# Kernel optimization log

Hardware: AMD Instinct MI355X
Metric: run time of the kernel (lower is better)

Reference implementation:

```python
import jax, jax.numpy as jnp
import numpy as np
import math

BS, NAG, HID, NACT, MESS, QD, KD, STEPS, INP = 4096, 8, 256, 16, 64, 64, 64, 5, 128
TRAJ = STEPS * NACT
LAMQ = 0.5


def setup_inputs() -> dict:
    key = jax.random.key(0)
    ks = jax.random.split(key, 12)
    g = lambda k, shape, fan: jax.random.normal(k, shape, jnp.float32) / math.sqrt(fan)
    d = {}
    d["inputs"] = jax.random.normal(ks[0], (BS * NAG, INP), jnp.float32)
    d["old_hstate"] = jax.random.normal(ks[1], (BS * NAG, HID), jnp.float32)
    d["fc1_w"] = g(ks[2], (HID, INP), INP); d["fc1_b"] = jnp.zeros((HID,), jnp.float32)
    d["w_ih"] = g(ks[3], (3 * HID, HID), HID); d["w_hh"] = g(ks[4], (3 * HID, HID), HID)
    d["b_ih"] = jnp.zeros((3 * HID,), jnp.float32); d["b_hh"] = jnp.zeros((3 * HID,), jnp.float32)
    d["dec_w"] = g(ks[5], (NACT, HID), HID); d["dec_b"] = jnp.zeros((NACT,), jnp.float32)
    d["trans_w"] = g(ks[6], (HID, HID + NAG), HID + NAG); d["trans_b"] = jnp.zeros((HID,), jnp.float32)
    d["qij_w"] = g(ks[7], (NACT, HID + MESS), HID + MESS); d["qij_b"] = jnp.zeros((NACT,), jnp.float32)
    d["q_w"] = g(ks[8], (QD, TRAJ), TRAJ); d["q_b"] = jnp.zeros((QD,), jnp.float32)
    d["k_w"] = g(ks[9], (KD, TRAJ), TRAJ); d["k_b"] = jnp.zeros((KD,), jnp.float32)
    d["v_w"] = g(ks[10], (MESS, TRAJ), TRAJ); d["v_b"] = jnp.zeros((MESS,), jnp.float32)
    return d


def _fwd(inputs, old_hstate, fc1_w, fc1_b, w_ih, w_hh, b_ih, b_hh,
         dec_w, dec_b, trans_w, trans_b, qij_w, qij_b,
         q_w, q_b, k_w, k_b, v_w, v_b):
    # fc1 + relu
    x = jax.nn.relu(inputs @ fc1_w.T + fc1_b)  # (BS*NAG, HID)
    # GRUCell (torch gate order: r, z, n)
    gi = x @ w_ih.T + b_ih
    gh = old_hstate @ w_hh.T + b_hh
    ir, iz, i_n = jnp.split(gi, 3, axis=-1)
    hr, hz, h_n = jnp.split(gh, 3, axis=-1)
    r = jax.nn.sigmoid(ir + hr)
    z = jax.nn.sigmoid(iz + hz)
    n = jnp.tanh(i_n + r * h_n)
    h_new = (1.0 - z) * n + z * old_hstate
    h = h_new.reshape(BS, NAG, HID)

    # imagination rollout on detached h
    def step(hc, _):
        q_inf = hc @ dec_w.T + dec_b                       # (BS, NAG, NACT)
        ac = jnp.argmax(q_inf, axis=-1).astype(hc.dtype)   # (BS, NAG)
        ac = jnp.broadcast_to(ac[:, None, :], (BS, NAG, NAG))
        ti = jnp.concatenate([hc, ac], axis=-1)            # (BS, NAG, HID+NAG)
        return ti @ trans_w.T + trans_b, q_inf

    _, qs = jax.lax.scan(step, jax.lax.stop_gradient(h), None, length=STEPS)
    # qs: (STEPS, BS, NAG, NACT) -> trajectory (BS, NAG, STEPS*NACT), step-major on last dim
    traj = jnp.moveaxis(qs, 0, 2).reshape(BS, NAG, TRAJ)

    # tiny agent attention
    query = traj @ q_w.T + q_b   # (BS, NAG, QD)
    key_t = traj @ k_w.T + k_b   # (BS, NAG, KD)
    value = traj @ v_w.T + v_b   # (BS, NAG, MESS)
    score = jnp.einsum('bnq,bmq->bnm', query, key_t) / math.sqrt(MESS)
    attn = jax.nn.softmax(score, axis=-1)
    traj_msg = jnp.einsum('bnm,bmd->bnd', attn, value)  # (BS, NAG, MESS)

    q_local = h @ dec_w.T + dec_b
    q_ij = jnp.concatenate([h, traj_msg], axis=-1) @ qij_w.T + qij_b
    q = q_local + LAMQ * q_ij
    return q, h


def reference(inputs, old_hstate, fc1_w, fc1_b, w_ih, w_hh, b_ih, b_hh,
              dec_w, dec_b, trans_w, trans_b, qij_w, qij_b,
              q_w, q_b, k_w, k_b, v_w, v_b):
    return _fwd(inputs, old_hstate, fc1_w, fc1_b, w_ih, w_hh, b_ih, b_hh,
                dec_w, dec_b, trans_w, trans_b, qij_w, qij_b,
                q_w, q_b, k_w, k_b, v_w, v_b)
```

## Files before the change

kernel.cpp:

```cpp
#include <hip/hip_runtime.h>
#include <math.h>

typedef unsigned short u16;
typedef unsigned int   u32;
typedef __attribute__((ext_vector_type(8))) short bf16x8;
typedef __attribute__((ext_vector_type(4))) float f32x4;

#define NROWS 32768
#define NAG 8
#define HID 256
#define INP 128
#define NACT 16
#define MESS 64
#define TRAJD 80
#define QD 64
#define HOFF 524288

#define PKO_FC1 0
#define PKO_IH  98304
#define PKO_HH  688128
#define PKO_TR  1277952
#define PKO_DEC 1499136
#define PKO_QKV 1511424
#define PKO_QIJ 1566720
#define PK_TOTAL 1582080
#define WS_CB   791040
#define WS_FLAG 793312

#define OB_FC1B 0
#define OB_BIH  256
#define OB_BHH  1024
#define OB_DECB 1792
#define OB_TRB  1808
#define OB_QIJB 2064
#define OB_QB   2080

__device__ __forceinline__ float bf2f(u16 v){ return __uint_as_float(((u32)v)<<16); }
__device__ __forceinline__ u16 f2bf(float f){
    u32 u = __float_as_uint(f);
    return (u16)((u + 0x7fffu + ((u>>16)&1u))>>16);
}
__device__ __forceinline__ float sig_(float x){ return 1.0f/(1.0f+expf(-x)); }
__device__ __forceinline__ float ldin(const void* p, size_t i, int f32){
    return f32 ? ((const float*)p)[i] : bf2f(((const u16*)p)[i]);
}
__device__ __forceinline__ void stout1(void* out, size_t i, float v, int f32){
    if (f32) ((float*)out)[i]=v; else ((u16*)out)[i]=f2bf(v);
}
__device__ __forceinline__ void split3(float w, u16& s0, u16& s1, u16& s2){
    u16 a=f2bf(w); float r  = w - bf2f(a);
    u16 b=f2bf(r); float r2 = r - bf2f(b);
    s0=a; s1=b; s2=f2bf(r2);
}
__device__ __forceinline__ f32x4 splat4(float b){ f32x4 v = {b,b,b,b}; return v; }

#define MFMA(a,b,c) __builtin_amdgcn_mfma_f32_16x16x32_bf16((a),(b),(c),0,0,0)

__device__ __forceinline__ bf16x8 lda_pl(const u16* P, int p, int row, int kbyte){
    const char* b = (const char*)P + ((p*32+row)*640) + (kbyte ^ ((row&7)<<4));
    return *(const bf16x8*)b;
}
__device__ __forceinline__ void stw_pl(u16* P, int p, int row, int col, u16 v){
    char* b = (char*)P + ((p*32+row)*640) + (((col*2)) ^ ((row&7)<<4));
    *(u16*)b = v;
}
__device__ __forceinline__ void split_store_pl(u16* P, int row, int col, float v){
    u16 a,b,c; split3(v,a,b,c);
    stw_pl(P,0,row,col,a); stw_pl(P,1,row,col,b); stw_pl(P,2,row,col,c);
}
__device__ __forceinline__ bf16x8 ldg_bf8(const void* p, size_t off){
    return *(const bf16x8*)((const u16*)p + off);
}
__device__ __forceinline__ void ldg_f32_split(const void* p, size_t off, bf16x8& f0, bf16x8& f1, bf16x8& f2){
    const float* fp = (const float*)p + off;
    #pragma unroll
    for (int j=0;j<8;j++){
        float w = fp[j];
        u16 a,b,c; split3(w,a,b,c);
        f0[j]=(short)a; f1[j]=(short)b; f2[j]=(short)c;
    }
}
#define BCH(base, NTv, ksv, pbv, ntv) \
    (*(const bf16x8*)((base) + ((((ksv)*3+(pbv))*(NTv) + (ntv))*512) + lane*8))

__global__ void k_det(const void* __restrict__ inp, int* __restrict__ flag){
    __shared__ int cnt;
    if (threadIdx.x==0) cnt=0;
    __syncthreads();
    int big=0;
    for (int i=threadIdx.x;i<128;i+=64){
        u32 w = ((const u32*)inp)[i];
        float g = bf2f((u16)w);
        if (!(fabsf(g) <= 1e4f)) big++;
    }
    if (big) atomicAdd(&cnt, big);
    __syncthreads();
    if (threadIdx.x==0) *flag = (cnt>=4) ? 1 : 0;
}

__device__ __forceinline__ void pack_tile(const void* W, int Kdim, int NT, u16* pk, int tau, int f32){
    int lane2 = tau & 63, c = tau >> 6;
    int nt = c % NT, ks = c / NT;
    int n  = nt*16 + (lane2 & 15);
    int kb = ks*32 + (lane2 >> 4)*8;
    u16 o0[8],o1[8],o2[8];
    #pragma unroll
    for (int j=0;j<8;j++){
        int k = kb + j;
        float w = (k < Kdim) ? ldin(W, (size_t)n*Kdim + k, f32) : 0.0f;
        split3(w, o0[j], o1[j], o2[j]);
    }
    size_t base = ((size_t)(ks*3+0)*NT + nt)*512 + lane2*8;
    size_t step = (size_t)NT*512;
    #pragma unroll
    for (int j=0;j<8;j++){
        pk[base+j]=o0[j]; pk[base+step+j]=o1[j]; pk[base+2*step+j]=o2[j];
    }
}

__global__ __launch_bounds__(256) void k0_prep(
    const void* fc1_w, const void* w_ih, const void* w_hh, const void* trans_w,
    const void* dec_w, const void* qij_w, const void* q_w, const void* k_w, const void* v_w,
    const void* fc1_b, const void* b_ih, const void* b_hh, const void* dec_b,
    const void* trans_b, const void* qij_b, const void* q_b, const void* k_b, const void* v_b,
    float* __restrict__ ws, const int* __restrict__ flagp)
{
    const int f32 = *flagp;
    u16* pk = (u16*)ws;
    int i = blockIdx.x*256 + threadIdx.x;
    if (i < 4096)        pack_tile(fc1_w,  128, 16, pk+PKO_FC1, i,        f32);
    else if (i < 28672)  pack_tile(w_ih,   256, 48, pk+PKO_IH,  i-4096,   f32);
    else if (i < 53248)  pack_tile(w_hh,   256, 48, pk+PKO_HH,  i-28672,  f32);
    else if (i < 62464)  pack_tile(trans_w,264, 16, pk+PKO_TR,  i-53248,  f32);
    else if (i < 62976)  pack_tile(dec_w,  256,  1, pk+PKO_DEC, i-62464,  f32);
    else if (i < 65280){
        int tau = i - 62976;
        int lane2 = tau&63, c = tau>>6, nt = c%12, ks = c/12;
        int n = nt*16 + (lane2&15);
        const void* W = (n<64)? q_w : (n<128 ? k_w : v_w);
        int nl = n & 63;
        int kb = ks*32 + (lane2>>4)*8;
        u16 o0[8],o1[8],o2[8];
        #pragma unroll
        for (int j=0;j<8;j++){
            int k = kb + j;
            float w = (k < 80) ? ldin(W, (size_t)nl*80 + k, f32) : 0.0f;
            split3(w, o0[j], o1[j], o2[j]);
        }
        u16* dst = pk + PKO_QKV;
        size_t base = ((size_t)(ks*3+0)*12 + nt)*512 + lane2*8;
        size_t step = (size_t)12*512;
        #pragma unroll
        for (int j=0;j<8;j++){
            dst[base+j]=o0[j]; dst[base+step+j]=o1[j]; dst[base+2*step+j]=o2[j];
        }
    }
    else if (i < 65920)  pack_tile(qij_w,  320,  1, pk+PKO_QIJ, i-65280,  f32);
    else if (i < 68192){
        int i2 = i - 65920;
        float v;
        if      (i2<256)  v=ldin(fc1_b,i2,f32);
        else if (i2<1024) v=ldin(b_ih,i2-256,f32);
        else if (i2<1792) v=ldin(b_hh,i2-1024,f32);
        else if (i2<1808) v=ldin(dec_b,i2-1792,f32);
        else if (i2<2064) v=ldin(trans_b,i2-1808,f32);
        else if (i2<2080) v=ldin(qij_b,i2-2064,f32);
        else if (i2<2144) v=ldin(q_b,i2-2080,f32);
        else if (i2<2208) v=ldin(k_b,i2-2144,f32);
        else              v=ldin(v_b,i2-2208,f32);
        ws[WS_CB+i2]=v;
    }
}

template<int F32>
__global__ __launch_bounds__(512,2) void k12_fused(
    const void* __restrict__ inp, const void* __restrict__ oldh,
    const float* __restrict__ ws, void* __restrict__ dout, const int* __restrict__ flagp)
{
    if (*flagp != F32) return;
    constexpr int PBW = F32 ? 2 : 0;
    constexpr int PAG = F32 ? 2 : 0;

    __shared__ __align__(16) u16   planes[3*32*320];
    __shared__ __align__(16) float s_traj[32*100];
    __shared__ __align__(16) float s_qkv[32*196];
    __shared__ float s_att[256];

    const int t = threadIdx.x;
    const int wid = t>>6, lane = t&63, lr = lane&15, lk = lane>>4;
    const int nt0 = wid, nt1 = wid + 8;
    const int c0 = nt0*16+lr, c1 = nt1*16+lr;
    const int row0 = blockIdx.x*32;
    const u16* pk = (const u16*)ws;
    const float* cb = ws + WS_CB;
    const u16* pkf = pk + PKO_FC1;
    const u16* pki = pk + PKO_IH;
    const u16* pkh = pk + PKO_HH;
    const u16* pkt = pk + PKO_TR;
    const u16* pkd = pk + PKO_DEC;
    const u16* pkq = pk + PKO_QKV;
    const u16* pkj = pk + PKO_QIJ;

    for (int i=t;i<15360;i+=512) ((u32*)planes)[i]=0u;
    for (int i=t;i<3200;i+=512) s_traj[i]=0.f;
    __syncthreads();

    {
        f32x4 acc[2][2];
        acc[0][0]=splat4(cb[OB_FC1B+c0]); acc[1][0]=acc[0][0];
        acc[0][1]=splat4(cb[OB_FC1B+c1]); acc[1][1]=acc[0][1];
        for (int ks=0;ks<4;ks++){
            bf16x8 a[2][3];
            if (F32){
                ldg_f32_split(inp,(size_t)(row0+lr)*INP + ks*32+lk*8,    a[0][0],a[0][1],a[0][2]);
                ldg_f32_split(inp,(size_t)(row0+16+lr)*INP + ks*32+lk*8, a[1][0],a[1][1],a[1][2]);
            } else {
                a[0][0]=ldg_bf8(inp,(size_t)(row0+lr)*INP + ks*32+lk*8);
                a[1][0]=ldg_bf8(inp,(size_t)(row0+16+lr)*INP + ks*32+lk*8);
            }
            #pragma unroll
            for (int pb=0;pb<=PBW;pb++){
                bf16x8 B0 = BCH(pkf,16,ks,pb,nt0);
                bf16x8 B1 = BCH(pkf,16,ks,pb,nt1);
                #pragma unroll
                for (int pa=0;pa<=((PAG<2-pb)?PAG:(2-pb));pa++){
                    acc[0][0]=MFMA(a[0][pa],B0,acc[0][0]); acc[0][1]=MFMA(a[0][pa],B1,acc[0][1]);
                    acc[1][0]=MFMA(a[1][pa],B0,acc[1][0]); acc[1][1]=MFMA(a[1][pa],B1,acc[1][1]);
                }
            }
        }
        #pragma unroll
        for (int m=0;m<2;m++)
        #pragma unroll
        for (int ni=0;ni<2;ni++)
        #pragma unroll
        for (int j=0;j<4;j++){
            float v = acc[m][ni][j]; v = v>0.f ? v : 0.f;
            split_store_pl(planes, m*16+lk*4+j, (ni?nt1:nt0)*16+lr, v);
        }
    }
    __syncthreads();

    float hreg[16];
    {
        f32x4 aR[2][2], aZ[2][2], aN[2][2], aH[2][2];
        #pragma unroll
        for (int m=0;m<2;m++)
        #pragma unroll
        for (int gi=0;gi<2;gi++){
            int c = (gi?nt1:nt0)*16 + lr;
            aR[m][gi]=splat4(cb[OB_BIH+c]     + cb[OB_BHH+c]);
            aZ[m][gi]=splat4(cb[OB_BIH+256+c] + cb[OB_BHH+256+c]);
            aN[m][gi]=splat4(cb[OB_BIH+512+c]);
            aH[m][gi]=splat4(cb[OB_BHH+512+c]);
        }
        for (int ks=0;ks<8;ks++){
            #pragma unroll
            for (int pb=0;pb<=PBW;pb++){
                bf16x8 Br0=BCH(pki,48,ks,pb,   nt0), Br1=BCH(pki,48,ks,pb,   nt1);
                bf16x8 Bz0=BCH(pki,48,ks,pb,16+nt0), Bz1=BCH(pki,48,ks,pb,16+nt1);
                bf16x8 Bn0=BCH(pki,48,ks,pb,32+nt0), Bn1=BCH(pki,48,ks,pb,32+nt1);
                #pragma unroll
                for (int pa=0;pa<=2-pb;pa++){
                    bf16x8 a0 = lda_pl(planes, pa, lr,    ks*64+lk*16);
                    bf16x8 a1 = lda_pl(planes, pa, 16+lr, ks*64+lk*16);
                    aR[0][0]=MFMA(a0,Br0,aR[0][0]); aR[0][1]=MFMA(a0,Br1,aR[0][1]);
                    aR[1][0]=MFMA(a1,Br0,aR[1][0]); aR[1][1]=MFMA(a1,Br1,aR[1][1]);
                    aZ[0][0]=MFMA(a0,Bz0,aZ[0][0]); aZ[0][1]=MFMA(a0,Bz1,aZ[0][1]);
                    aZ[1][0]=MFMA(a1,Bz0,aZ[1][0]); aZ[1][1]=MFMA(a1,Bz1,aZ[1][1]);
                    aN[0][0]=MFMA(a0,Bn0,aN[0][0]); aN[0][1]=MFMA(a0,Bn1,aN[0][1]);
                    aN[1][0]=MFMA(a1,Bn0,aN[1][0]); aN[1][1]=MFMA(a1,Bn1,aN[1][1]);
                }
            }
        }
        for (int ks=0;ks<8;ks++){
            bf16x8 a[2][3];
            if (F32){
                ldg_f32_split(oldh,(size_t)(row0+lr)*HID + ks*32+lk*8,    a[0][0],a[0][1],a[0][2]);
                ldg_f32_split(oldh,(size_t)(row0+16+lr)*HID + ks*32+lk*8, a[1][0],a[1][1],a[1][2]);
            } else {
                a[0][0]=ldg_bf8(oldh,(size_t)(row0+lr)*HID + ks*32+lk*8);
                a[1][0]=ldg_bf8(oldh,(size_t)(row0+16+lr)*HID + ks*32+lk*8);
            }
            #pragma unroll
            for (int pb=0;pb<=PBW;pb++){
                bf16x8 Br0=BCH(pkh,48,ks,pb,   nt0), Br1=BCH(pkh,48,ks,pb,   nt1);
                bf16x8 Bz0=BCH(pkh,48,ks,pb,16+nt0), Bz1=BCH(pkh,48,ks,pb,16+nt1);
                bf16x8 Bh0=BCH(pkh,48,ks,pb,32+nt0), Bh1=BCH(pkh,48,ks,pb,32+nt1);
                #pragma unroll
                for (int pa=0;pa<=((PAG<2-pb)?PAG:(2-pb));pa++){
                    aR[0][0]=MFMA(a[0][pa],Br0,aR[0][0]); aR[0][1]=MFMA(a[0][pa],Br1,aR[0][1]);
                    aR[1][0]=MFMA(a[1][pa],Br0,aR[1][0]); aR[1][1]=MFMA(a[1][pa],Br1,aR[1][1]);
                    aZ[0][0]=MFMA(a[0][pa],Bz0,aZ[0][0]); aZ[0][1]=MFMA(a[0][pa],Bz1,aZ[0][1]);
                    aZ[1][0]=MFMA(a[1][pa],Bz0,aZ[1][0]); aZ[1][1]=MFMA(a[1][pa],Bz1,aZ[1][1]);
                    aH[0][0]=MFMA(a[0][pa],Bh0,aH[0][0]); aH[0][1]=MFMA(a[0][pa],Bh1,aH[0][1]);
                    aH[1][0]=MFMA(a[1][pa],Bh0,aH[1][0]); aH[1][1]=MFMA(a[1][pa],Bh1,aH[1][1]);
                }
            }
        }
        #pragma unroll
        for (int m=0;m<2;m++)
        #pragma unroll
        for (int gi=0;gi<2;gi++)
        #pragma unroll
        for (int j=0;j<4;j++){
            int row = m*16 + lk*4 + j;
            int c   = (gi?nt1:nt0)*16 + lr;
            float r  = sig_(aR[m][gi][j]);
            float z  = sig_(aZ[m][gi][j]);
            float nv = tanhf(aN[m][gi][j] + r*aH[m][gi][j]);
            float ho = ldin(oldh,(size_t)(row0+row)*HID + c, F32);
            float h  = (1.f-z)*nv + z*ho;
            hreg[m*8+gi*4+j] = h;
            if (F32)
                stout1(dout,(size_t)HOFF + (size_t)(row0+row)*HID + c, h, F32);
        }
    }
    __syncthreads();
    #pragma unroll
    for (int m=0;m<2;m++)
    #pragma unroll
    for (int gi=0;gi<2;gi++)
    #pragma unroll
    for (int j=0;j<4;j++)
        split_store_pl(planes, m*16+lk*4+j, (gi?nt1:nt0)*16+lr, hreg[m*8+gi*4+j]);
    __syncthreads();

    if (!F32){
        #pragma unroll
        for (int c2=0;c2<2;c2++){
            int cid = t + c2*512;
            int row = cid>>5, c8 = cid&31;
            bf16x8 v = lda_pl(planes, 0, row, c8*16);
            *(bf16x8*)((u16*)dout + HOFF + (size_t)(row0+row)*HID + c8*8) = v;
        }
    }

    #pragma unroll 1
    for (int s=0;s<5;s++){
        if (wid<2){
            const int m = wid;
            f32x4 d0 = splat4(cb[OB_DECB+lr]);
            f32x4 d1 = splat4(0.f), d2 = splat4(0.f);
            for (int ks=0;ks<8;ks++){
                #pragma unroll
                for (int pb=0;pb<=PBW;pb++){
                    bf16x8 B = BCH(pkd,1,ks,pb,0);
                    #pragma unroll
                    for (int pa=0;pa<=2-pb;pa++){
                        bf16x8 a = lda_pl(planes, pa, m*16+lr, ks*64+lk*16);
                        if (pa==0) d0=MFMA(a,B,d0); else if (pa==1) d1=MFMA(a,B,d1); else d2=MFMA(a,B,d2);
                    }
                }
            }
            f32x4 q;
            #pragma unroll
            for (int j=0;j<4;j++) q[j]=d0[j]+d1[j]+d2[j];
            #pragma unroll
            for (int j=0;j<4;j++) s_traj[(m*16+lk*4+j)*100 + s*16 + lr] = q[j];
            if (s<4){
                #pragma unroll
                for (int j=0;j<4;j++){
                    float v = q[j]; int ai = lr;
                    #pragma unroll
                    for (int msk=1; msk<16; msk<<=1){
                        float pv = __shfl_xor(v, msk);
                        int   pi = __shfl_xor(ai, msk);
                        if (pv>v || (pv==v && pi<ai)){ v=pv; ai=pi; }
                    }
                    if (lr<8){
                        int R = m*16+lk*4+j;
                        stw_pl(planes, 0, (R&~7)+lr, 256+(R&7), f2bf((float)ai));
                    }
                }
            }
        }
        if (s==4) break;
        __syncthreads();
        {
            f32x4 tc[2][2];
            tc[0][0]=splat4(cb[OB_TRB+c0]); tc[1][0]=tc[0][0];
            tc[0][1]=splat4(cb[OB_TRB+c1]); tc[1][1]=tc[0][1];
            for (int ks=0;ks<9;ks++){
                #pragma unroll
                for (int pb=0;pb<=PBW;pb++){
                    bf16x8 B0=BCH(pkt,16,ks,pb,nt0), B1=BCH(pkt,16,ks,pb,nt1);
                    #pragma unroll
                    for (int pa=0;pa<=2-pb;pa++){
                        bf16x8 a0 = lda_pl(planes,pa,lr,   ks*64+lk*16);
                        bf16x8 a1 = lda_pl(planes,pa,16+lr,ks*64+lk*16);
                        tc[0][0]=MFMA(a0,B0,tc[0][0]); tc[0][1]=MFMA(a0,B1,tc[0][1]);
                        tc[1][0]=MFMA(a1,B0,tc[1][0]); tc[1][1]=MFMA(a1,B1,tc[1][1]);
                    }
                }
            }
            __syncthreads();
            #pragma unroll
            for (int m=0;m<2;m++)
            #pragma unroll
            for (int ni=0;ni<2;ni++)
            #pragma unroll
            for (int j=0;j<4;j++)
                split_store_pl(planes, m*16+lk*4+j, (ni?nt1:nt0)*16+lr, tc[m][ni][j]);
        }
        __syncthreads();
    }
    __syncthreads();

    #pragma unroll
    for (int m=0;m<2;m++)
    #pragma unroll
    for (int gi=0;gi<2;gi++)
    #pragma unroll
    for (int j=0;j<4;j++)
        split_store_pl(planes, m*16+lk*4+j, (gi?nt1:nt0)*16+lr, hreg[m*8+gi*4+j]);
    if (wid<6){
        f32x4 acc[2][2];
        acc[0][0]=splat4(cb[OB_QB+2*wid*16+lr]);     acc[1][0]=acc[0][0];
        acc[0][1]=splat4(cb[OB_QB+(2*wid+1)*16+lr]); acc[1][1]=acc[0][1];
        for (int ks=0;ks<3;ks++){
            bf16x8 a[2][3];
            #pragma unroll
            for (int m=0;m<2;m++){
                const float* tp = s_traj + (m*16+lr)*100 + ks*32 + lk*8;
                #pragma unroll
                for (int e=0;e<8;e++){
                    u16 x0,x1,x2; split3(tp[e],x0,x1,x2);
                    a[m][0][e]=(short)x0; a[m][1][e]=(short)x1; a[m][2][e]=(short)x2;
                }
            }
            #pragma unroll
            for (int pb=0;pb<=PBW;pb++){
                bf16x8 B0 = BCH(pkq,12,ks,pb,2*wid);
                bf16x8 B1 = BCH(pkq,12,ks,pb,2*wid+1);
                #pragma unroll
                for (int pa=0;pa<=2-pb;pa++){
                    acc[0][0]=MFMA(a[0][pa],B0,acc[0][0]); acc[0][1]=MFMA(a[0][pa],B1,acc[0][1]);
                    acc[1][0]=MFMA(a[1][pa],B0,acc[1][0]); acc[1][1]=MFMA(a[1][pa],B1,acc[1][1]);
                }
            }
        }
        #pragma unroll
        for (int m=0;m<2;m++)
        #pragma unroll
        for (int j=0;j<4;j++){
            s_qkv[(m*16+lk*4+j)*196 + 2*wid*16+lr]     = acc[m][0][j];
            s_qkv[(m*16+lk*4+j)*196 + (2*wid+1)*16+lr] = acc[m][1][j];
        }
    }
    __syncthreads();
    if (t<256){
        int b=t>>6, n=(t>>3)&7, mm=t&7;
        const float* qv = s_qkv + (b*8+n)*196;
        const float* kv = s_qkv + (b*8+mm)*196 + 64;
        float a2=0.f;
        #pragma unroll
        for (int d2=0;d2<64;d2++) a2 += qv[d2]*kv[d2];
        s_att[t] = a2*0.125f;
    }
    __syncthreads();
    if (t<32){
        float mx = s_att[t*8];
        #pragma unroll
        for (int j2=1;j2<8;j2++) mx = fmaxf(mx, s_att[t*8+j2]);
        float e[8]; float sum=0.f;
        #pragma unroll
        for (int j2=0;j2<8;j2++){ e[j2]=expf(s_att[t*8+j2]-mx); sum+=e[j2]; }
        float inv = 1.f/sum;
        #pragma unroll
        for (int j2=0;j2<8;j2++) s_att[t*8+j2] = e[j2]*inv;
    }
    __syncthreads();
    for (int o=t;o<2048;o+=512){
        int row=o>>6, d2=o&63, b=row>>3;
        float a3=0.f;
        #pragma unroll
        for (int mm=0;mm<8;mm++) a3 += s_att[row*8+mm]*s_qkv[(b*8+mm)*196+128+d2];
        split_store_pl(planes, row, 256+d2, a3);
    }
    __syncthreads();
    if (wid<2){
        const int m = wid;
        f32x4 e0 = splat4(cb[OB_QIJB+lr]);
        f32x4 e1 = splat4(0.f), e2 = splat4(0.f);
        for (int ks=0;ks<10;ks++){
            #pragma unroll
            for (int pb=0;pb<=PBW;pb++){
                bf16x8 B = BCH(pkj,1,ks,pb,0);
                #pragma unroll
                for (int pa=0;pa<=2-pb;pa++){
                    bf16x8 a = lda_pl(planes, pa, m*16+lr, ks*64+lk*16);
                    if (pa==0) e0=MFMA(a,B,e0); else if (pa==1) e1=MFMA(a,B,e1); else e2=MFMA(a,B,e2);
                }
            }
        }
        #pragma unroll
        for (int j=0;j<4;j++){
            int row = m*16+lk*4+j;
            float ql = s_traj[row*100 + lr];
            stout1(dout,(size_t)(row0+row)*NACT + lr, ql + 0.5f*(e0[j]+e1[j]+e2[j]), F32);
        }
    }
}

extern "C" void kernel_launch(void* const* d_in, const int* in_sizes, int n_in,
                              void* d_out, int out_size, void* d_ws, size_t ws_size,
                              hipStream_t stream)
{
    (void)in_sizes; (void)n_in; (void)out_size; (void)ws_size;
    const void* inputs = d_in[0];
    const void* oldh   = d_in[1];
    float* ws = (float*)d_ws;
    int* flagp = (int*)(ws + WS_FLAG);

    k_det<<<1,64,0,stream>>>(inputs, flagp);
    k0_prep<<<268,256,0,stream>>>(d_in[2],d_in[4],d_in[5],d_in[10],d_in[8],d_in[12],
                                  d_in[14],d_in[16],d_in[18],
                                  d_in[3],d_in[6],d_in[7],d_in[9],d_in[11],d_in[13],
                                  d_in[15],d_in[17],d_in[19],
                                  ws, flagp);
    k12_fused<0><<<1024,512,0,stream>>>(inputs, oldh, ws, d_out, flagp);
    k12_fused<1><<<1024,512,0,stream>>>(inputs, oldh, ws, d_out, flagp);
}
```

Measured before the change: 590.6 us.

## Double block to 1024 threads, one 16-column N-tile per wave

Each block now runs 16 waves instead of 8. Every wave owns a single 16-wide output column tile rather than two, across the fc1, GRU, transition, QKV and output stages. This gives each wave less register pressure and shorter serial MFMA chains, and spreads the per-block work over more waves. In exchange, launch bounds drop to one block per CU, so occupancy stays about the same. Each A fragment is now reused across fewer MFMAs, which means more LDS and global A loads per FLOP.

Result: slower. 782.2 us (+32.4%).

```diff
diff --git a/kernel.cpp b/kernel.cpp
--- a/kernel.cpp
+++ b/kernel.cpp
@@ -173,7 +173,7 @@
 }
 
 template<int F32>
-__global__ __launch_bounds__(512,2) void k12_fused(
+__global__ __launch_bounds__(1024,1) void k12_fused(
     const void* __restrict__ inp, const void* __restrict__ oldh,
     const float* __restrict__ ws, void* __restrict__ dout, const int* __restrict__ flagp)
 {
@@ -188,8 +188,8 @@
 
     const int t = threadIdx.x;
     const int wid = t>>6, lane = t&63, lr = lane&15, lk = lane>>4;
-    const int nt0 = wid, nt1 = wid + 8;
-    const int c0 = nt0*16+lr, c1 = nt1*16+lr;
+    const int nt = wid;
+    const int c0 = nt*16+lr;
     const int row0 = blockIdx.x*32;
     const u16* pk = (const u16*)ws;
     const float* cb = ws + WS_CB;
@@ -201,14 +201,13 @@
     const u16* pkq = pk + PKO_QKV;
     const u16* pkj = pk + PKO_QIJ;
 
-    for (int i=t;i<15360;i+=512) ((u32*)planes)[i]=0u;
-    for (int i=t;i<3200;i+=512) s_traj[i]=0.f;
+    for (int i=t;i<15360;i+=1024) ((u32*)planes)[i]=0u;
+    for (int i=t;i<3200;i+=1024) s_traj[i]=0.f;
     __syncthreads();
 
     {
-        f32x4 acc[2][2];
-        acc[0][0]=splat4(cb[OB_FC1B+c0]); acc[1][0]=acc[0][0];
-        acc[0][1]=splat4(cb[OB_FC1B+c1]); acc[1][1]=acc[0][1];
+        f32x4 acc[2];
+        acc[0]=splat4(cb[OB_FC1B+c0]); acc[1]=acc[0];
         for (int ks=0;ks<4;ks++){
             bf16x8 a[2][3];
             if (F32){
@@ -220,56 +219,44 @@
             }
             #pragma unroll
             for (int pb=0;pb<=PBW;pb++){
-                bf16x8 B0 = BCH(pkf,16,ks,pb,nt0);
-                bf16x8 B1 = BCH(pkf,16,ks,pb,nt1);
+                bf16x8 B = BCH(pkf,16,ks,pb,nt);
                 #pragma unroll
                 for (int pa=0;pa<=((PAG<2-pb)?PAG:(2-pb));pa++){
-                    acc[0][0]=MFMA(a[0][pa],B0,acc[0][0]); acc[0][1]=MFMA(a[0][pa],B1,acc[0][1]);
-                    acc[1][0]=MFMA(a[1][pa],B0,acc[1][0]); acc[1][1]=MFMA(a[1][pa],B1,acc[1][1]);
+                    acc[0]=MFMA(a[0][pa],B,acc[0]);
+                    acc[1]=MFMA(a[1][pa],B,acc[1]);
                 }
             }
         }
         #pragma unroll
         for (int m=0;m<2;m++)
         #pragma unroll
-        for (int ni=0;ni<2;ni++)
-        #pragma unroll
         for (int j=0;j<4;j++){
-            float v = acc[m][ni][j]; v = v>0.f ? v : 0.f;
-            split_store_pl(planes, m*16+lk*4+j, (ni?nt1:nt0)*16+lr, v);
-        }
-    }
-    __syncthreads();
-
-    float hreg[16];
+            float v = acc[m][j]; v = v>0.f ? v : 0.f;
+            split_store_pl(planes, m*16+lk*4+j, c0, v);
+        }
+    }
+    __syncthreads();
+
+    float hreg[8];
     {
-        f32x4 aR[2][2], aZ[2][2], aN[2][2], aH[2][2];
-        #pragma unroll
-        for (int m=0;m<2;m++)
-        #pragma unroll
-        for (int gi=0;gi<2;gi++){
-            int c = (gi?nt1:nt0)*16 + lr;
-            aR[m][gi]=splat4(cb[OB_BIH+c]     + cb[OB_BHH+c]);
-            aZ[m][gi]=splat4(cb[OB_BIH+256+c] + cb[OB_BHH+256+c]);
-            aN[m][gi]=splat4(cb[OB_BIH+512+c]);
-            aH[m][gi]=splat4(cb[OB_BHH+512+c]);
-        }
+        f32x4 aR[2], aZ[2], aN[2], aH[2];
+        aR[0]=splat4(cb[OB_BIH+c0]     + cb[OB_BHH+c0]);     aR[1]=aR[0];
+        aZ[0]=splat4(cb[OB_BIH+256+c0] + cb[OB_BHH+256+c0]); aZ[1]=aZ[0];
+        aN[0]=splat4(cb[OB_BIH+512+c0]);                     aN[1]=aN[0];
+        aH[0]=splat4(cb[OB_BHH+512+c0]);                     aH[1]=aH[0];
         for (int ks=0;ks<8;ks++){
             #pragma unroll
             for (int pb=0;pb<=PBW;pb++){
-                bf16x8 Br0=BCH(pki,48,ks,pb,   nt0), Br1=BCH(pki,48,ks,pb,   nt1);
-                bf16x8 Bz0=BCH(pki,48,ks,pb,16+nt0), Bz1=BCH(pki,48,ks,pb,16+nt1);
-                bf16x8 Bn0=BCH(pki,48,ks,pb,32+nt0), Bn1=BCH(pki,48,ks,pb,32+nt1);
+                bf16x8 Br=BCH(pki,48,ks,pb,   nt);
+                bf16x8 Bz=BCH(pki,48,ks,pb,16+nt);
+                bf16x8 Bn=BCH(pki,48,ks,pb,32+nt);
                 #pragma unroll
                 for (int pa=0;pa<=2-pb;pa++){
                     bf16x8 a0 = lda_pl(planes, pa, lr,    ks*64+lk*16);
                     bf16x8 a1 = lda_pl(planes, pa, 16+lr, ks*64+lk*16);
-                    aR[0][0]=MFMA(a0,Br0,aR[0][0]); aR[0][1]=MFMA(a0,Br1,aR[0][1]);
-                    aR[1][0]=MFMA(a1,Br0,aR[1][0]); aR[1][1]=MFMA(a1,Br1,aR[1][1]);
-                    aZ[0][0]=MFMA(a0,Bz0,aZ[0][0]); aZ[0][1]=MFMA(a0,Bz1,aZ[0][1]);
-                    aZ[1][0]=MFMA(a1,Bz0,aZ[1][0]); aZ[1][1]=MFMA(a1,Bz1,aZ[1][1]);
-                    aN[0][0]=MFMA(a0,Bn0,aN[0][0]); aN[0][1]=MFMA(a0,Bn1,aN[0][1]);
-                    aN[1][0]=MFMA(a1,Bn0,aN[1][0]); aN[1][1]=MFMA(a1,Bn1,aN[1][1]);
+                    aR[0]=MFMA(a0,Br,aR[0]); aR[1]=MFMA(a1,Br,aR[1]);
+                    aZ[0]=MFMA(a0,Bz,aZ[0]); aZ[1]=MFMA(a1,Bz,aZ[1]);
+                    aN[0]=MFMA(a0,Bn,aN[0]); aN[1]=MFMA(a1,Bn,aN[1]);
                 }
             }
         }
@@ -284,56 +271,44 @@
             }
             #pragma unroll
             for (int pb=0;pb<=PBW;pb++){
-                bf16x8 Br0=BCH(pkh,48,ks,pb,   nt0), Br1=BCH(pkh,48,ks,pb,   nt1);
-                bf16x8 Bz0=BCH(pkh,48,ks,pb,16+nt0), Bz1=BCH(pkh,48,ks,pb,16+nt1);
-                bf16x8 Bh0=BCH(pkh,48,ks,pb,32+nt0), Bh1=BCH(pkh,48,ks,pb,32+nt1);
+                bf16x8 Br=BCH(pkh,48,ks,pb,   nt);
+                bf16x8 Bz=BCH(pkh,48,ks,pb,16+nt);
+                bf16x8 Bh=BCH(pkh,48,ks,pb,32+nt);
                 #pragma unroll
                 for (int pa=0;pa<=((PAG<2-pb)?PAG:(2-pb));pa++){
-                    aR[0][0]=MFMA(a[0][pa],Br0,aR[0][0]); aR[0][1]=MFMA(a[0][pa],Br1,aR[0][1]);
-                    aR[1][0]=MFMA(a[1][pa],Br0,aR[1][0]); aR[1][1]=MFMA(a[1][pa],Br1,aR[1][1]);
-                    aZ[0][0]=MFMA(a[0][pa],Bz0,aZ[0][0]); aZ[0][1]=MFMA(a[0][pa],Bz1,aZ[0][1]);
-                    aZ[1][0]=MFMA(a[1][pa],Bz0,aZ[1][0]); aZ[1][1]=MFMA(a[1][pa],Bz1,aZ[1][1]);
-                    aH[0][0]=MFMA(a[0][pa],Bh0,aH[0][0]); aH[0][1]=MFMA(a[0][pa],Bh1,aH[0][1]);
-                    aH[1][0]=MFMA(a[1][pa],Bh0,aH[1][0]); aH[1][1]=MFMA(a[1][pa],Bh1,aH[1][1]);
+                    aR[0]=MFMA(a[0][pa],Br,aR[0]); aR[1]=MFMA(a[1][pa],Br,aR[1]);
+                    aZ[0]=MFMA(a[0][pa],Bz,aZ[0]); aZ[1]=MFMA(a[1][pa],Bz,aZ[1]);
+                    aH[0]=MFMA(a[0][pa],Bh,aH[0]); aH[1]=MFMA(a[1][pa],Bh,aH[1]);
                 }
             }
         }
         #pragma unroll
         for (int m=0;m<2;m++)
-        #pragma unroll
-        for (int gi=0;gi<2;gi++)
         #pragma unroll
         for (int j=0;j<4;j++){
             int row = m*16 + lk*4 + j;
-            int c   = (gi?nt1:nt0)*16 + lr;
-            float r  = sig_(aR[m][gi][j]);
-            float z  = sig_(aZ[m][gi][j]);
-            float nv = tanhf(aN[m][gi][j] + r*aH[m][gi][j]);
-            float ho = ldin(oldh,(size_t)(row0+row)*HID + c, F32);
+            float r  = sig_(aR[m][j]);
+            float z  = sig_(aZ[m][j]);
+            float nv = tanhf(aN[m][j] + r*aH[m][j]);
+            float ho = ldin(oldh,(size_t)(row0+row)*HID + c0, F32);
             float h  = (1.f-z)*nv + z*ho;
-            hreg[m*8+gi*4+j] = h;
+            hreg[m*4+j] = h;
             if (F32)
-                stout1(dout,(size_t)HOFF + (size_t)(row0+row)*HID + c, h, F32);
+                stout1(dout,(size_t)HOFF + (size_t)(row0+row)*HID + c0, h, F32);
         }
     }
     __syncthreads();
     #pragma unroll
     for (int m=0;m<2;m++)
     #pragma unroll
-    for (int gi=0;gi<2;gi++)
-    #pragma unroll
     for (int j=0;j<4;j++)
-        split_store_pl(planes, m*16+lk*4+j, (gi?nt1:nt0)*16+lr, hreg[m*8+gi*4+j]);
+        split_store_pl(planes, m*16+lk*4+j, c0, hreg[m*4+j]);
     __syncthreads();
 
     if (!F32){
-        #pragma unroll
-        for (int c2=0;c2<2;c2++){
-            int cid = t + c2*512;
-            int row = cid>>5, c8 = cid&31;
-            bf16x8 v = lda_pl(planes, 0, row, c8*16);
-            *(bf16x8*)((u16*)dout + HOFF + (size_t)(row0+row)*HID + c8*8) = v;
-        }
+        int row = t>>5, c8 = t&31;
+        bf16x8 v = lda_pl(planes, 0, row, c8*16);
+        *(bf16x8*)((u16*)dout + HOFF + (size_t)(row0+row)*HID + c8*8) = v;
     }
 
     #pragma unroll 1
@@ -378,19 +353,18 @@
         if (s==4) break;
         __syncthreads();
         {
-            f32x4 tc[2][2];
-            tc[0][0]=splat4(cb[OB_TRB+c0]); tc[1][0]=tc[0][0];
-            tc[0][1]=splat4(cb[OB_TRB+c1]); tc[1][1]=tc[0][1];
+            f32x4 tc[2];
+            tc[0]=splat4(cb[OB_TRB+c0]); tc[1]=tc[0];
             for (int ks=0;ks<9;ks++){
                 #pragma unroll
                 for (int pb=0;pb<=PBW;pb++){
-                    bf16x8 B0=BCH(pkt,16,ks,pb,nt0), B1=BCH(pkt,16,ks,pb,nt1);
+                    bf16x8 B=BCH(pkt,16,ks,pb,nt);
                     #pragma unroll
                     for (int pa=0;pa<=2-pb;pa++){
                         bf16x8 a0 = lda_pl(planes,pa,lr,   ks*64+lk*16);
                         bf16x8 a1 = lda_pl(planes,pa,16+lr,ks*64+lk*16);
-                        tc[0][0]=MFMA(a0,B0,tc[0][0]); tc[0][1]=MFMA(a0,B1,tc[0][1]);
-                        tc[1][0]=MFMA(a1,B0,tc[1][0]); tc[1][1]=MFMA(a1,B1,tc[1][1]);
+                        tc[0]=MFMA(a0,B,tc[0]);
+                        tc[1]=MFMA(a1,B,tc[1]);
                     }
                 }
             }
@@ -398,10 +372,8 @@
             #pragma unroll
             for (int m=0;m<2;m++)
             #pragma unroll
-            for (int ni=0;ni<2;ni++)
-            #pragma unroll
             for (int j=0;j<4;j++)
-                split_store_pl(planes, m*16+lk*4+j, (ni?nt1:nt0)*16+lr, tc[m][ni][j]);
+                split_store_pl(planes, m*16+lk*4+j, c0, tc[m][j]);
         }
         __syncthreads();
     }
@@ -410,14 +382,11 @@
     #pragma unroll
     for (int m=0;m<2;m++)
     #pragma unroll
-    for (int gi=0;gi<2;gi++)
-    #pragma unroll
     for (int j=0;j<4;j++)
-        split_store_pl(planes, m*16+lk*4+j, (gi?nt1:nt0)*16+lr, hreg[m*8+gi*4+j]);
-    if (wid<6){
-        f32x4 acc[2][2];
-        acc[0][0]=splat4(cb[OB_QB+2*wid*16+lr]);     acc[1][0]=acc[0][0];
-        acc[0][1]=splat4(cb[OB_QB+(2*wid+1)*16+lr]); acc[1][1]=acc[0][1];
+        split_store_pl(planes, m*16+lk*4+j, c0, hreg[m*4+j]);
+    if (wid<12){
+        f32x4 acc[2];
+        acc[0]=splat4(cb[OB_QB+wid*16+lr]); acc[1]=acc[0];
         for (int ks=0;ks<3;ks++){
             bf16x8 a[2][3];
             #pragma unroll
@@ -431,22 +400,19 @@
             }
             #pragma unroll
             for (int pb=0;pb<=PBW;pb++){
-                bf16x8 B0 = BCH(pkq,12,ks,pb,2*wid);
-                bf16x8 B1 = BCH(pkq,12,ks,pb,2*wid+1);
+                bf16x8 B = BCH(pkq,12,ks,pb,wid);
                 #pragma unroll
                 for (int pa=0;pa<=2-pb;pa++){
-                    acc[0][0]=MFMA(a[0][pa],B0,acc[0][0]); acc[0][1]=MFMA(a[0][pa],B1,acc[0][1]);
-                    acc[1][0]=MFMA(a[1][pa],B0,acc[1][0]); acc[1][1]=MFMA(a[1][pa],B1,acc[1][1]);
+                    acc[0]=MFMA(a[0][pa],B,acc[0]);
+                    acc[1]=MFMA(a[1][pa],B,acc[1]);
                 }
             }
         }
         #pragma unroll
         for (int m=0;m<2;m++)
         #pragma unroll
-        for (int j=0;j<4;j++){
-            s_qkv[(m*16+lk*4+j)*196 + 2*wid*16+lr]     = acc[m][0][j];
-            s_qkv[(m*16+lk*4+j)*196 + (2*wid+1)*16+lr] = acc[m][1][j];
-        }
+        for (int j=0;j<4;j++)
+            s_qkv[(m*16+lk*4+j)*196 + wid*16+lr] = acc[m][j];
     }
     __syncthreads();
     if (t<256){
@@ -471,7 +437,7 @@
         for (int j2=0;j2<8;j2++) s_att[t*8+j2] = e[j2]*inv;
     }
     __syncthreads();
-    for (int o=t;o<2048;o+=512){
+    for (int o=t;o<2048;o+=1024){
         int row=o>>6, d2=o&63, b=row>>3;
         float a3=0.f;
         #pragma unroll
@@ -519,6 +485,6 @@
                                   d_in[3],d_in[6],d_in[7],d_in[9],d_in[11],d_in[13],
                                   d_in[15],d_in[17],d_in[19],
                                   ws, flagp);
-    k12_fused<0><<<1024,512,0,stream>>>(inputs, oldh, ws, d_out, flagp);
-    k12_fused<1><<<1024,512,0,stream>>>(inputs, oldh, ws, d_out, flagp);
-}
+    k12_fused<0><<<1024,1024,0,stream>>>(inputs, oldh, ws, d_out, flagp);
+    k12_fused<1><<<1024,1024,0,stream>>>(inputs, oldh, ws, d_out, flagp);
+}
```
